# Kernel optimization log

Measured on AMD Instinct MI355X. Metric: run time of the kernel, lower is better.

## Reference

```python
import jax, jax.numpy as jnp
import numpy as np

B, T, D = 8, 2048, 1024
E, S = 8, 1            # num_experts, num_slots
FF = 4 * (S * D)       # ffn_mult * (num_slots * hiddens)

def setup_inputs() -> dict:
    key = jax.random.key(0)
    ks = jax.random.split(key, 7)
    sd = S * D
    inp = {
        "X":  jax.random.normal(ks[0], (B, T, D), dtype=jnp.float32),
        # slots gating MLP (single linear D -> E*S)
        "Wg": jax.random.normal(ks[1], (D, E * S), dtype=jnp.float32) / np.sqrt(D),
        "bg": jnp.zeros((E * S,), dtype=jnp.float32),
        # expert FFN (weights SHARED across experts, as in source [FFN(...)]*E)
        "W1": jax.random.normal(ks[2], (sd, FF), dtype=jnp.float32) / np.sqrt(sd),
        "b1": jnp.zeros((FF,), dtype=jnp.float32),
        "W2": jax.random.normal(ks[3], (FF, sd), dtype=jnp.float32) / np.sqrt(FF),
        "b2": jnp.zeros((sd,), dtype=jnp.float32),
    }
    return inp

def reference(X, Wg, bg, W1, b1, W2, b2):
    # logits: (B, T, E*S)
    logits = jnp.einsum('btd,de->bte', X, Wg) + bg
    dispatch_w = jax.nn.softmax(logits, axis=1)   # over tokens T
    combine_w = jax.nn.softmax(logits, axis=2)    # over slots E*S
    # slots = dispatch_w^T @ X : (B, E*S, D) -> (B, E, S*D)
    slots = jnp.einsum('bte,btd->bed', dispatch_w, X).reshape(B, E, S * D)
    # shared-weight FFN applied per expert slot (dropout=0 at eval)
    h = jax.nn.silu(jnp.einsum('bef,fh->beh', slots, W1) + b1)
    y = jnp.einsum('beh,hf->bef', h, W2) + b2     # (B, E, S*D)
    y = y.reshape(B, E * S, D)
    # combine: (B, T, E*S) @ (B, E*S, D)
    return jnp.einsum('bte,bed->btd', combine_w, y)
```

## Files before the change

### kernel.cpp

```cpp
#include <hip/hip_runtime.h>
#include <math.h>

#define B_  8
#define T_  2048
#define D_  1024
#define E_  8
#define FF_ 4096
#define N_  64
#define BT_ (B_*T_)

#define LPART_F  0u
#define HACC_F   0u
#define H_F      262144u
#define SPART_F  1048576u

__global__ __launch_bounds__(256) void k_logits_part(
    const float* __restrict__ X, const float* __restrict__ Wg,
    float* __restrict__ part)
{
    __shared__ float xt[256 * 36];

    const int tid = threadIdx.x;
    const int bt0 = blockIdx.x * 256;
    const int d0  = blockIdx.y * 128;

    float acc[8];
    #pragma unroll
    for (int e = 0; e < 8; ++e) acc[e] = 0.f;

    for (int dt = 0; dt < 4; ++dt) {
        if (dt) __syncthreads();
        #pragma unroll
        for (int r = 0; r < 8; ++r) {
            int fi = r * 256 + tid;
            int token = fi >> 3, dj = fi & 7;
            const float4 v = *(const float4*)
                &X[(size_t)(bt0 + token) * D_ + d0 + dt * 32 + dj * 4];
            *(float4*)&xt[token * 36 + dj * 4] = v;
        }
        __syncthreads();
        #pragma unroll
        for (int dj = 0; dj < 8; ++dj) {
            const float4 x4 = *(const float4*)&xt[tid * 36 + dj * 4];
            const int db = d0 + dt * 32 + dj * 4;
            const float xv[4] = {x4.x, x4.y, x4.z, x4.w};
            #pragma unroll
            for (int r = 0; r < 4; ++r) {
                const float4 wlo = *(const float4*)&Wg[(size_t)(db + r) * 8];
                const float4 whi = *(const float4*)&Wg[(size_t)(db + r) * 8 + 4];
                acc[0] += xv[r] * wlo.x; acc[1] += xv[r] * wlo.y;
                acc[2] += xv[r] * wlo.z; acc[3] += xv[r] * wlo.w;
                acc[4] += xv[r] * whi.x; acc[5] += xv[r] * whi.y;
                acc[6] += xv[r] * whi.z; acc[7] += xv[r] * whi.w;
            }
        }
    }

    float* pp = &part[LPART_F + (size_t)blockIdx.y * BT_ * E_
                      + (size_t)(bt0 + tid) * E_];
    *(float4*)&pp[0] = make_float4(acc[0], acc[1], acc[2], acc[3]);
    *(float4*)&pp[4] = make_float4(acc[4], acc[5], acc[6], acc[7]);
}

__global__ __launch_bounds__(256) void k_logits_merge(
    const float* __restrict__ part, const float* __restrict__ bg,
    float* __restrict__ logits, float* __restrict__ sexp_part)
{
    __shared__ float red[8 * 256];
    const int tid = threadIdx.x;
    const int token = blockIdx.x * 256 + tid;

    float a[8];
    #pragma unroll
    for (int e = 0; e < 8; ++e) a[e] = 0.f;
    #pragma unroll
    for (int p = 0; p < 8; ++p) {
        const float* pp = &part[LPART_F + (size_t)p * BT_ * E_
                                + (size_t)token * E_];
        const float4 v0 = *(const float4*)&pp[0];
        const float4 v1 = *(const float4*)&pp[4];
        a[0] += v0.x; a[1] += v0.y; a[2] += v0.z; a[3] += v0.w;
        a[4] += v1.x; a[5] += v1.y; a[6] += v1.z; a[7] += v1.w;
    }
    #pragma unroll
    for (int e = 0; e < 8; ++e) a[e] += bg[e];

    float* lp = &logits[(size_t)token * E_];
    *(float4*)&lp[0] = make_float4(a[0], a[1], a[2], a[3]);
    *(float4*)&lp[4] = make_float4(a[4], a[5], a[6], a[7]);

    #pragma unroll
    for (int e = 0; e < 8; ++e) red[e * 256 + tid] = expf(a[e]);
    __syncthreads();
    for (int s = 128; s >= 1; s >>= 1) {
        if (tid < s) {
            #pragma unroll
            for (int e = 0; e < 8; ++e)
                red[e * 256 + tid] += red[e * 256 + tid + s];
        }
        __syncthreads();
    }
    if (tid < 8) sexp_part[blockIdx.x * 8 + tid] = red[tid * 256];
}

__global__ __launch_bounds__(256) void k_slots_part(
    const float* __restrict__ X, const float* __restrict__ logits,
    const float* __restrict__ sexp_part, float* __restrict__ part)
{
    __shared__ float wlds[32 * 8];
    __shared__ float red[64];
    __shared__ float inv[8];

    const int tid = threadIdx.x;
    const int ts = blockIdx.x, b = blockIdx.y;
    const int t0 = ts * 32;

    if (tid < 64) red[tid] = sexp_part[b * 64 + tid];
    __syncthreads();
    if (tid < 8) {
        float s = 0.f;
        #pragma unroll
        for (int i = 0; i < 8; ++i) s += red[i * 8 + tid];
        inv[tid] = 1.f / s;
    }
    __syncthreads();
    {
        int t = tid >> 3, e = tid & 7;
        wlds[tid] = expf(logits[((size_t)b * T_ + t0 + t) * E_ + e]) * inv[e];
    }
    __syncthreads();

    float4 acc[8];
    #pragma unroll
    for (int e = 0; e < 8; ++e) acc[e] = make_float4(0.f, 0.f, 0.f, 0.f);

    const float* xb = &X[((size_t)b * T_ + t0) * D_ + tid * 4];
    #pragma unroll 8
    for (int t = 0; t < 32; ++t) {
        const float4 x4 = *(const float4*)&xb[(size_t)t * D_];
        const float4 wA = *(const float4*)&wlds[t * 8];
        const float4 wB = *(const float4*)&wlds[t * 8 + 4];
        const float w[8] = {wA.x, wA.y, wA.z, wA.w, wB.x, wB.y, wB.z, wB.w};
        #pragma unroll
        for (int e = 0; e < 8; ++e) {
            acc[e].x += x4.x * w[e];
            acc[e].y += x4.y * w[e];
            acc[e].z += x4.z * w[e];
            acc[e].w += x4.w * w[e];
        }
    }
    #pragma unroll
    for (int e = 0; e < 8; ++e) {
        *(float4*)&part[SPART_F + (size_t)ts * (N_ * D_)
                        + (size_t)(b * E_ + e) * D_ + tid * 4] = acc[e];
    }
}

__global__ __launch_bounds__(256) void k_reduce_slots(
    const float* __restrict__ part, float* __restrict__ slots)
{
    const int i = blockIdx.x * 256 + threadIdx.x;
    float s = 0.f;
    #pragma unroll
    for (int p = 0; p < 64; ++p)
        s += part[SPART_F + (size_t)p * (N_ * D_) + i];
    slots[i] = s;
}

template<int K, int F>
__global__ __launch_bounds__(256) void k_gemm_atomic(
    const float* __restrict__ A, const float* __restrict__ W,
    float* __restrict__ outp)
{
    __shared__ float As[64 * 132];

    const int tid = threadIdx.x;
    const int rg = tid >> 4, cg = tid & 15;
    const int f0 = blockIdx.x * 64 + cg * 4;
    const int k0 = blockIdx.y * 128;

    #pragma unroll
    for (int i = 0; i < 8; ++i) {
        int idx = i * 256 + tid;
        int row = idx >> 5, kq = idx & 31;
        *(float4*)&As[row * 132 + kq * 4] =
            *(const float4*)&A[(size_t)row * K + k0 + kq * 4];
    }
    __syncthreads();

    float4 acc[4];
    #pragma unroll
    for (int r = 0; r < 4; ++r) acc[r] = make_float4(0.f, 0.f, 0.f, 0.f);

    #pragma unroll 2
    for (int kq = 0; kq < 32; ++kq) {
        const float* wr = &W[(size_t)(k0 + kq * 4) * F + f0];
        const float4 w0 = *(const float4*)&wr[0];
        const float4 w1 = *(const float4*)&wr[(size_t)F];
        const float4 w2 = *(const float4*)&wr[2 * (size_t)F];
        const float4 w3 = *(const float4*)&wr[3 * (size_t)F];
        #pragma unroll
        for (int r = 0; r < 4; ++r) {
            const float4 a = *(const float4*)&As[(rg * 4 + r) * 132 + kq * 4];
            acc[r].x += a.x*w0.x + a.y*w1.x + a.z*w2.x + a.w*w3.x;
            acc[r].y += a.x*w0.y + a.y*w1.y + a.z*w2.y + a.w*w3.y;
            acc[r].z += a.x*w0.z + a.y*w1.z + a.z*w2.z + a.w*w3.z;
            acc[r].w += a.x*w0.w + a.y*w1.w + a.z*w2.w + a.w*w3.w;
        }
    }

    #pragma unroll
    for (int r = 0; r < 4; ++r) {
        float* op = &outp[(size_t)(rg * 4 + r) * F + f0];
        unsafeAtomicAdd(&op[0], acc[r].x);
        unsafeAtomicAdd(&op[1], acc[r].y);
        unsafeAtomicAdd(&op[2], acc[r].z);
        unsafeAtomicAdd(&op[3], acc[r].w);
    }
}

__global__ __launch_bounds__(256) void k_silu(
    const float* __restrict__ hacc, const float* __restrict__ b1,
    float* __restrict__ h)
{
    const int i4 = blockIdx.x * 256 + threadIdx.x;
    const float4 v = *(const float4*)&hacc[(size_t)i4 * 4];
    const float4 bb = *(const float4*)&b1[(i4 * 4) & (FF_ - 1)];
    float4 r;
    r.x = v.x + bb.x; r.y = v.y + bb.y; r.z = v.z + bb.z; r.w = v.w + bb.w;
    r.x = r.x / (1.f + expf(-r.x));
    r.y = r.y / (1.f + expf(-r.y));
    r.z = r.z / (1.f + expf(-r.z));
    r.w = r.w / (1.f + expf(-r.w));
    *(float4*)&h[(size_t)i4 * 4] = r;
}

__global__ __launch_bounds__(256) void k_combine(
    const float* __restrict__ logits, const float* __restrict__ yacc,
    const float* __restrict__ b2, float* __restrict__ out)
{
    __shared__ float wlds[64 * 8];
    const int tid = threadIdx.x;
    const int dc = blockIdx.x, tc = blockIdx.y, b = blockIdx.z;
    const int t0 = tc * 64;

    if (tid < 64) {
        const float* lp = &logits[((size_t)b * T_ + t0 + tid) * E_];
        float ex[8]; float s = 0.f;
        #pragma unroll
        for (int i = 0; i < 8; ++i) { ex[i] = expf(lp[i]); s += ex[i]; }
        const float invs = 1.f / s;
        #pragma unroll
        for (int i = 0; i < 8; ++i) wlds[tid * 8 + i] = ex[i] * invs;
    }
    __syncthreads();

    const int d = dc * 256 + tid;
    const float bv = b2[d];
    float yv[8];
    #pragma unroll
    for (int e = 0; e < 8; ++e)
        yv[e] = yacc[(size_t)(b * E_ + e) * D_ + d] + bv;

    for (int t = 0; t < 64; ++t) {
        const float4 wA = *(const float4*)&wlds[t * 8];
        const float4 wB = *(const float4*)&wlds[t * 8 + 4];
        const float acc = wA.x*yv[0] + wA.y*yv[1] + wA.z*yv[2] + wA.w*yv[3]
                        + wB.x*yv[4] + wB.y*yv[5] + wB.z*yv[6] + wB.w*yv[7];
        out[((size_t)b * T_ + t0 + t) * D_ + d] = acc;
    }
}

extern "C" void kernel_launch(void* const* d_in, const int* in_sizes, int n_in,
                              void* d_out, int out_size, void* d_ws, size_t ws_size,
                              hipStream_t stream)
{
    const float* X  = (const float*)d_in[0];
    const float* Wg = (const float*)d_in[1];
    const float* bg = (const float*)d_in[2];
    const float* W1 = (const float*)d_in[3];
    const float* b1 = (const float*)d_in[4];
    const float* W2 = (const float*)d_in[5];
    const float* b2 = (const float*)d_in[6];
    float* out = (float*)d_out;

    float* wsf       = (float*)d_ws;
    float* logits    = wsf;
    float* sexp_part = logits + BT_ * E_;
    float* slots     = sexp_part + 512;
    float* yacc      = slots + N_ * D_;

    float* hacc = out + HACC_F;
    float* h    = out + H_F;

    hipLaunchKernelGGL(k_logits_part,  dim3(BT_ / 256, 8), dim3(256), 0, stream,
                       X, Wg, out);
    hipLaunchKernelGGL(k_logits_merge, dim3(BT_ / 256),    dim3(256), 0, stream,
                       out, bg, logits, sexp_part);
    hipLaunchKernelGGL(k_slots_part,   dim3(64, 8),        dim3(256), 0, stream,
                       X, logits, sexp_part, out);
    hipLaunchKernelGGL(k_reduce_slots, dim3(256),          dim3(256), 0, stream,
                       out, slots);
    hipMemsetAsync(hacc, 0, (size_t)N_ * FF_ * sizeof(float), stream);
    hipMemsetAsync(yacc, 0, (size_t)N_ * D_ * sizeof(float), stream);
    hipLaunchKernelGGL((k_gemm_atomic<1024, 4096>), dim3(FF_ / 64, 1024 / 128),
                       dim3(256), 0, stream, slots, W1, hacc);
    hipLaunchKernelGGL(k_silu,         dim3(N_ * FF_ / 1024), dim3(256), 0, stream,
                       hacc, b1, h);
    hipLaunchKernelGGL((k_gemm_atomic<4096, 1024>), dim3(D_ / 64, FF_ / 128),
                       dim3(256), 0, stream, h, W2, yacc);
    hipLaunchKernelGGL(k_combine,      dim3(4, 32, 8), dim3(256), 0, stream,
                       logits, yacc, b2, out);
}
```

Measured before the change: 285.2 us.

## Replace atomic split-K FFN GEMMs with partial-buffer split-K and fused reductions

The two FFN GEMMs drop atomic accumulation and the two memsets. Each block now owns a 64x16 output tile and walks a much larger K range, storing float4 partials into scratch space in the output buffer. Separate kernels then sum the partials: one adds b1 and applies SiLU, the other adds b2, so k_combine no longer adds the bias. Each thread now does one row instead of four, so every weight load feeds a single row of FMAs. This cuts A-reuse per W load and may raise weight traffic in exchange for removing atomics.

```diff
diff --git a/kernel.cpp b/kernel.cpp
--- a/kernel.cpp
+++ b/kernel.cpp
@@ -10,9 +10,9 @@
 #define BT_ (B_*T_)
 
 #define LPART_F  0u
-#define HACC_F   0u
-#define H_F      262144u
 #define SPART_F  1048576u
+#define G1PART_F 5242880u
+#define G2PART_F 5767168u
 
 __global__ __launch_bounds__(256) void k_logits_part(
     const float* __restrict__ X, const float* __restrict__ Wg,
@@ -167,67 +167,61 @@
     slots[i] = s;
 }
 
-template<int K, int F>
-__global__ __launch_bounds__(256) void k_gemm_atomic(
+template<int K, int F, int KSPLIT>
+__global__ __launch_bounds__(256, 2) void k_ffn(
     const float* __restrict__ A, const float* __restrict__ W,
-    float* __restrict__ outp)
+    float* __restrict__ part)
 {
     __shared__ float As[64 * 132];
 
     const int tid = threadIdx.x;
-    const int rg = tid >> 4, cg = tid & 15;
-    const int f0 = blockIdx.x * 64 + cg * 4;
-    const int k0 = blockIdx.y * 128;
-
-    #pragma unroll
-    for (int i = 0; i < 8; ++i) {
-        int idx = i * 256 + tid;
-        int row = idx >> 5, kq = idx & 31;
-        *(float4*)&As[row * 132 + kq * 4] =
-            *(const float4*)&A[(size_t)row * K + k0 + kq * 4];
-    }
-    __syncthreads();
-
-    float4 acc[4];
-    #pragma unroll
-    for (int r = 0; r < 4; ++r) acc[r] = make_float4(0.f, 0.f, 0.f, 0.f);
-
-    #pragma unroll 2
-    for (int kq = 0; kq < 32; ++kq) {
-        const float* wr = &W[(size_t)(k0 + kq * 4) * F + f0];
-        const float4 w0 = *(const float4*)&wr[0];
-        const float4 w1 = *(const float4*)&wr[(size_t)F];
-        const float4 w2 = *(const float4*)&wr[2 * (size_t)F];
-        const float4 w3 = *(const float4*)&wr[3 * (size_t)F];
-        #pragma unroll
-        for (int r = 0; r < 4; ++r) {
-            const float4 a = *(const float4*)&As[(rg * 4 + r) * 132 + kq * 4];
-            acc[r].x += a.x*w0.x + a.y*w1.x + a.z*w2.x + a.w*w3.x;
-            acc[r].y += a.x*w0.y + a.y*w1.y + a.z*w2.y + a.w*w3.y;
-            acc[r].z += a.x*w0.z + a.y*w1.z + a.z*w2.z + a.w*w3.z;
-            acc[r].w += a.x*w0.w + a.y*w1.w + a.z*w2.w + a.w*w3.w;
-        }
-    }
-
-    #pragma unroll
-    for (int r = 0; r < 4; ++r) {
-        float* op = &outp[(size_t)(rg * 4 + r) * F + f0];
-        unsafeAtomicAdd(&op[0], acc[r].x);
-        unsafeAtomicAdd(&op[1], acc[r].y);
-        unsafeAtomicAdd(&op[2], acc[r].z);
-        unsafeAtomicAdd(&op[3], acc[r].w);
-    }
-}
-
-__global__ __launch_bounds__(256) void k_silu(
-    const float* __restrict__ hacc, const float* __restrict__ b1,
+    const int row = tid >> 2;
+    const int cg  = tid & 3;
+    const int f0  = blockIdx.x * 16 + cg * 4;
+    const int k0  = blockIdx.y * (K / KSPLIT);
+
+    float4 acc = make_float4(0.f, 0.f, 0.f, 0.f);
+
+    for (int c = 0; c < (K / KSPLIT) / 128; ++c) {
+        const int kb = k0 + c * 128;
+        if (c) __syncthreads();
+        #pragma unroll
+        for (int i = 0; i < 8; ++i) {
+            int idx = i * 256 + tid;
+            int r = idx >> 5, kq = idx & 31;
+            *(float4*)&As[r * 132 + kq * 4] =
+                *(const float4*)&A[(size_t)r * K + kb + kq * 4];
+        }
+        __syncthreads();
+        #pragma unroll 4
+        for (int kq = 0; kq < 32; ++kq) {
+            const float* wr = &W[(size_t)(kb + kq * 4) * F + f0];
+            const float4 w0 = *(const float4*)&wr[0];
+            const float4 w1 = *(const float4*)&wr[(size_t)F];
+            const float4 w2 = *(const float4*)&wr[2 * (size_t)F];
+            const float4 w3 = *(const float4*)&wr[3 * (size_t)F];
+            const float4 a = *(const float4*)&As[row * 132 + kq * 4];
+            acc.x += a.x*w0.x + a.y*w1.x + a.z*w2.x + a.w*w3.x;
+            acc.y += a.x*w0.y + a.y*w1.y + a.z*w2.y + a.w*w3.y;
+            acc.z += a.x*w0.z + a.y*w1.z + a.z*w2.z + a.w*w3.z;
+            acc.w += a.x*w0.w + a.y*w1.w + a.z*w2.w + a.w*w3.w;
+        }
+    }
+
+    *(float4*)&part[(size_t)blockIdx.y * (N_ * F) + (size_t)row * F + f0] = acc;
+}
+
+__global__ __launch_bounds__(256) void k_reduce_silu(
+    const float* __restrict__ part, const float* __restrict__ b1,
     float* __restrict__ h)
 {
     const int i4 = blockIdx.x * 256 + threadIdx.x;
-    const float4 v = *(const float4*)&hacc[(size_t)i4 * 4];
-    const float4 bb = *(const float4*)&b1[(i4 * 4) & (FF_ - 1)];
+    const float4 v0 = *(const float4*)&part[G1PART_F + (size_t)i4 * 4];
+    const float4 v1 = *(const float4*)&part[G1PART_F + (size_t)(N_ * FF_) + (size_t)i4 * 4];
+    const float4 bb = *(const float4*)&b1[(i4 & (FF_ / 4 - 1)) * 4];
     float4 r;
-    r.x = v.x + bb.x; r.y = v.y + bb.y; r.z = v.z + bb.z; r.w = v.w + bb.w;
+    r.x = v0.x + v1.x + bb.x; r.y = v0.y + v1.y + bb.y;
+    r.z = v0.z + v1.z + bb.z; r.w = v0.w + v1.w + bb.w;
     r.x = r.x / (1.f + expf(-r.x));
     r.y = r.y / (1.f + expf(-r.y));
     r.z = r.z / (1.f + expf(-r.z));
@@ -235,9 +229,25 @@
     *(float4*)&h[(size_t)i4 * 4] = r;
 }
 
+__global__ __launch_bounds__(256) void k_reduce_bias(
+    const float* __restrict__ part, const float* __restrict__ b2,
+    float* __restrict__ y)
+{
+    const int i4 = blockIdx.x * 256 + threadIdx.x;
+    const float4 bb = *(const float4*)&b2[(i4 & (D_ / 4 - 1)) * 4];
+    float4 r = bb;
+    #pragma unroll
+    for (int p = 0; p < 8; ++p) {
+        const float4 v = *(const float4*)
+            &part[G2PART_F + (size_t)p * (N_ * D_) + (size_t)i4 * 4];
+        r.x += v.x; r.y += v.y; r.z += v.z; r.w += v.w;
+    }
+    *(float4*)&y[(size_t)i4 * 4] = r;
+}
+
 __global__ __launch_bounds__(256) void k_combine(
-    const float* __restrict__ logits, const float* __restrict__ yacc,
-    const float* __restrict__ b2, float* __restrict__ out)
+    const float* __restrict__ logits, const float* __restrict__ y,
+    float* __restrict__ out)
 {
     __shared__ float wlds[64 * 8];
     const int tid = threadIdx.x;
@@ -256,11 +266,9 @@
     __syncthreads();
 
     const int d = dc * 256 + tid;
-    const float bv = b2[d];
     float yv[8];
     #pragma unroll
-    for (int e = 0; e < 8; ++e)
-        yv[e] = yacc[(size_t)(b * E_ + e) * D_ + d] + bv;
+    for (int e = 0; e < 8; ++e) yv[e] = y[(size_t)(b * E_ + e) * D_ + d];
 
     for (int t = 0; t < 64; ++t) {
         const float4 wA = *(const float4*)&wlds[t * 8];
@@ -288,10 +296,8 @@
     float* logits    = wsf;
     float* sexp_part = logits + BT_ * E_;
     float* slots     = sexp_part + 512;
-    float* yacc      = slots + N_ * D_;
-
-    float* hacc = out + HACC_F;
-    float* h    = out + H_F;
+    float* h         = slots + N_ * D_;
+    float* y         = h + N_ * FF_;
 
     hipLaunchKernelGGL(k_logits_part,  dim3(BT_ / 256, 8), dim3(256), 0, stream,
                        X, Wg, out);
@@ -301,14 +307,14 @@
                        X, logits, sexp_part, out);
     hipLaunchKernelGGL(k_reduce_slots, dim3(256),          dim3(256), 0, stream,
                        out, slots);
-    hipMemsetAsync(hacc, 0, (size_t)N_ * FF_ * sizeof(float), stream);
-    hipMemsetAsync(yacc, 0, (size_t)N_ * D_ * sizeof(float), stream);
-    hipLaunchKernelGGL((k_gemm_atomic<1024, 4096>), dim3(FF_ / 64, 1024 / 128),
-                       dim3(256), 0, stream, slots, W1, hacc);
-    hipLaunchKernelGGL(k_silu,         dim3(N_ * FF_ / 1024), dim3(256), 0, stream,
-                       hacc, b1, h);
-    hipLaunchKernelGGL((k_gemm_atomic<4096, 1024>), dim3(D_ / 64, FF_ / 128),
-                       dim3(256), 0, stream, h, W2, yacc);
+    hipLaunchKernelGGL((k_ffn<1024, 4096, 2>), dim3(FF_ / 16, 2), dim3(256), 0,
+                       stream, slots, W1, out + G1PART_F);
+    hipLaunchKernelGGL(k_reduce_silu,  dim3(256), dim3(256), 0, stream,
+                       out, b1, h);
+    hipLaunchKernelGGL((k_ffn<4096, 1024, 8>), dim3(D_ / 16, 8), dim3(256), 0,
+                       stream, h, W2, out + G2PART_F);
+    hipLaunchKernelGGL(k_reduce_bias,  dim3(64), dim3(256), 0, stream,
+                       out, b2, y);
     hipLaunchKernelGGL(k_combine,      dim3(4, 32, 8), dim3(256), 0, stream,
-                       logits, yacc, b2, out);
-}
+                       logits, y, out);
+}
```

Measured after the change: 284.3 us. Within noise of the previous version (-0.3%).
